# Optimization experiments

Measured on AMD Instinct MI355X. Metric: run time of the kernel, lower is better.

## Reference

```python
import jax, jax.numpy as jnp
import numpy as np

N, E, B = 20000, 60000, 800
H = 64          # node_out_feats
EOUT = 64       # edge_out_feats
D = H + EOUT    # set2set input dim = 128
NT = 138        # n_tasks


def _forward(node_feats, edge_feats, fp_vector, src, dst, gid,
             Wn, bn, We1, be1, We2, be2, Wres, Wgx, bgx, Wgh, bgh,
             Wep, bep,
             Wlx0, Wlh0, bl0, Wlx1, Wlh1, bl1, Wlx2, Wlh2, bl2,
             Wfp, bfp, bn_g, bn_b, bn_m, bn_v,
             Wf1, bf1, Wf2, bf2, Wp, bp):
    # ---- CustomMPNNGNN (dgllife MPNNGNN: proj + NNConv(edge-net) + GRU) ----
    h = jax.nn.relu(node_feats @ Wn + bn)                       # [N,64]
    We = jax.nn.relu(edge_feats @ We1 + be1) @ We2 + be2        # [E,4096]
    We = We.reshape(-1, H, H)                                   # [E,64,64] per-edge weight
    hs = h                                                      # GRU hidden state
    for _ in range(3):
        msg = jnp.einsum('ei,eio->eo', h[src], We)              # edge gather + matvec
        agg = jax.ops.segment_sum(msg, dst, num_segments=N)     # scatter-add to dst
        m = jax.nn.relu(agg + h @ Wres)                         # residual root weight
        gx = m @ Wgx + bgx
        gh = hs @ Wgh + bgh
        xr, xz, xn = jnp.split(gx, 3, axis=-1)
        hr, hz, hn = jnp.split(gh, 3, axis=-1)
        r = jax.nn.sigmoid(xr + hr)
        z = jax.nn.sigmoid(xz + hz)
        n = jnp.tanh(xn + r * hn)
        hs = (1.0 - z) * n + z * hs
        h = hs
    # ---- _internal_readout: gather src node emb + projected edge emb, segment-sum at dst ----
    e_emb = jax.nn.relu(edge_feats @ Wep + bep)                 # [E,64]
    src_msg = jnp.concatenate([h[src], e_emb], axis=1)          # [E,128]
    feat = jax.ops.segment_sum(src_msg, dst, num_segments=N)    # [N,128]
    # ---- Set2Set (3-layer LSTM hidden 128, 6 iterations) ----
    q_star = jnp.zeros((B, 2 * D), feat.dtype)
    hc = [(jnp.zeros((B, D), feat.dtype), jnp.zeros((B, D), feat.dtype)) for _ in range(3)]
    lstm = [(Wlx0, Wlh0, bl0), (Wlx1, Wlh1, bl1), (Wlx2, Wlh2, bl2)]
    for _ in range(6):
        x = q_star
        new_hc = []
        for (Wx, Wh, b), (hl, cl) in zip(lstm, hc):
            g = x @ Wx + hl @ Wh + b                            # [B,512] gates i,f,g,o
            gi, gf, gg, go = jnp.split(g, 4, axis=-1)
            cl = jax.nn.sigmoid(gf) * cl + jax.nn.sigmoid(gi) * jnp.tanh(gg)
            hl = jax.nn.sigmoid(go) * jnp.tanh(cl)
            new_hc.append((hl, cl))
            x = hl
        hc = new_hc
        q = x                                                   # [B,128]
        e = jnp.sum(feat * q[gid], axis=-1)                     # [N]
        emax = jax.ops.segment_max(e, gid, num_segments=B)
        a = jnp.exp(e - emax[gid])
        denom = jax.ops.segment_sum(a, gid, num_segments=B)
        alpha = a / (denom[gid] + 1e-9)
        r = jax.ops.segment_sum(alpha[:, None] * feat, gid, num_segments=B)  # [B,128]
        q_star = jnp.concatenate([q, r], axis=1)                # [B,256]
    # ---- Fingerprint encoder: Linear + BatchNorm1d(eval) + ReLU ----
    fp = fp_vector @ Wfp + bfp
    fp = jax.nn.relu((fp - bn_m) * bn_g * jax.lax.rsqrt(bn_v + 1e-5) + bn_b)  # [B,128]
    # ---- combined FFN (384 -> 300 -> 256) + prediction head ----
    comb = jnp.concatenate([q_star, fp], axis=1)                # [B,384]
    emb = jax.nn.relu(comb @ Wf1 + bf1) @ Wf2 + bf2             # [B,256]
    out = jax.nn.relu(emb) @ Wp + bp                            # [B,138]
    return out


def setup_inputs() -> dict:
    key = jax.random.key(0)
    ks = iter(jax.random.split(key, 64))
    def nrm(shape, s):
        return jax.random.normal(next(ks), shape, jnp.float32) * s
    inp = {}
    inp['node_feats'] = jax.random.normal(next(ks), (N, 134), jnp.float32)
    inp['edge_feats'] = jax.random.uniform(next(ks), (E, 6), jnp.float32)
    inp['fp_vector'] = jax.random.uniform(next(ks), (B, 1024), jnp.float32)
    inp['src'] = jax.random.randint(next(ks), (E,), 0, N)
    inp['dst'] = jax.random.randint(next(ks), (E,), 0, N)
    inp['gid'] = jnp.sort(jax.random.randint(next(ks), (N,), 0, B))
    # MPNN params
    inp['Wn'] = nrm((134, H), 0.08); inp['bn'] = jnp.zeros((H,), jnp.float32)
    inp['We1'] = nrm((6, 128), 0.2); inp['be1'] = jnp.zeros((128,), jnp.float32)
    inp['We2'] = nrm((128, H * H), 0.05); inp['be2'] = jnp.zeros((H * H,), jnp.float32)
    inp['Wres'] = nrm((H, H), 0.1)
    inp['Wgx'] = nrm((H, 3 * H), 0.1); inp['bgx'] = jnp.zeros((3 * H,), jnp.float32)
    inp['Wgh'] = nrm((H, 3 * H), 0.1); inp['bgh'] = jnp.zeros((3 * H,), jnp.float32)
    # edge projection for readout
    inp['Wep'] = nrm((6, EOUT), 0.2); inp['bep'] = jnp.zeros((EOUT,), jnp.float32)
    # Set2Set LSTM (layer0 input 2D=256, layers 1-2 input D=128, hidden D=128)
    inp['Wlx0'] = nrm((2 * D, 4 * D), 0.06); inp['Wlh0'] = nrm((D, 4 * D), 0.06); inp['bl0'] = jnp.zeros((4 * D,), jnp.float32)
    inp['Wlx1'] = nrm((D, 4 * D), 0.06); inp['Wlh1'] = nrm((D, 4 * D), 0.06); inp['bl1'] = jnp.zeros((4 * D,), jnp.float32)
    inp['Wlx2'] = nrm((D, 4 * D), 0.06); inp['Wlh2'] = nrm((D, 4 * D), 0.06); inp['bl2'] = jnp.zeros((4 * D,), jnp.float32)
    # fingerprint encoder
    inp['Wfp'] = nrm((1024, 128), 0.03); inp['bfp'] = jnp.zeros((128,), jnp.float32)
    inp['bn_g'] = jnp.ones((128,), jnp.float32); inp['bn_b'] = jnp.zeros((128,), jnp.float32)
    inp['bn_m'] = jnp.zeros((128,), jnp.float32); inp['bn_v'] = jnp.ones((128,), jnp.float32)
    # combined FFN + prediction head
    inp['Wf1'] = nrm((2 * D + 128, 300), 0.06); inp['bf1'] = jnp.zeros((300,), jnp.float32)
    inp['Wf2'] = nrm((300, 256), 0.06); inp['bf2'] = jnp.zeros((256,), jnp.float32)
    inp['Wp'] = nrm((256, NT), 0.06); inp['bp'] = jnp.zeros((NT,), jnp.float32)
    return inp


def reference(node_feats, edge_feats, fp_vector, src, dst, gid,
              Wn, bn, We1, be1, We2, be2, Wres, Wgx, bgx, Wgh, bgh,
              Wep, bep,
              Wlx0, Wlh0, bl0, Wlx1, Wlh1, bl1, Wlx2, Wlh2, bl2,
              Wfp, bfp, bn_g, bn_b, bn_m, bn_v,
              Wf1, bf1, Wf2, bf2, Wp, bp):
    return _forward(node_feats, edge_feats, fp_vector, src, dst, gid,
                    Wn, bn, We1, be1, We2, be2, Wres, Wgx, bgx, Wgh, bgh,
                    Wep, bep,
                    Wlx0, Wlh0, bl0, Wlx1, Wlh1, bl1, Wlx2, Wlh2, bl2,
                    Wfp, bfp, bn_g, bn_b, bn_m, bn_v,
                    Wf1, bf1, Wf2, bf2, Wp, bp)
```

## Files before the change

### kernel.cpp

```cpp
#include <hip/hip_runtime.h>

typedef short short8 __attribute__((ext_vector_type(8)));
typedef float f32x4  __attribute__((ext_vector_type(4)));

#define NN 20000
#define NE 60000
#define NB 800
#define NTASK 138
#define EB 128
#define EPAD 60032

#define O_WX0 0
#define O_WH0 131072
#define O_WX1 196608
#define O_WH1 262144
#define O_WX2 327680
#define O_WH2 393216
#define O_WF1 458752
#define O_WF2 573952
#define O_WP  650752
#define NWB   686080

static __device__ __forceinline__ float sigm(float x) { return 1.f / (1.f + expf(-x)); }

static __device__ __forceinline__ unsigned short f2bf(float x) {
    unsigned u = __float_as_uint(x);
    unsigned r = (u + 0x7fffu + ((u >> 16) & 1u)) >> 16;
    return (unsigned short)r;
}
static __device__ __forceinline__ float bf2f(unsigned short b) {
    return __uint_as_float(((unsigned)b) << 16);
}

__global__ void kpre(float* __restrict__ zbase, int nz4,
                     const float* __restrict__ We2, const float* __restrict__ be2,
                     unsigned short* __restrict__ thi,
                     const int* __restrict__ gid, int* __restrict__ seg,
                     const float* __restrict__ fpv, const float* __restrict__ Wfp,
                     const float* __restrict__ bfpv,
                     const float* __restrict__ bng, const float* __restrict__ bnb,
                     const float* __restrict__ bnm, const float* __restrict__ bnv,
                     float* __restrict__ fpb,
                     const float* __restrict__ nf, const float* __restrict__ Wn,
                     const float* __restrict__ bn, float* __restrict__ hf,
                     unsigned short* __restrict__ hb,
                     const float* __restrict__ ef, const float* __restrict__ We1,
                     const float* __restrict__ be1, float* __restrict__ xt,
                     const float* __restrict__ Wlx0, const float* __restrict__ Wlh0,
                     const float* __restrict__ Wlx1, const float* __restrict__ Wlh1,
                     const float* __restrict__ Wlx2, const float* __restrict__ Wlh2,
                     const float* __restrict__ Wf1, const float* __restrict__ Wf2,
                     const float* __restrict__ Wp, unsigned short* __restrict__ wb,
                     int B0, int B1, int B2, int B3, int B4, int B5) {
    __shared__ float st[64 * 65];
    __shared__ float sNF[16 * 134];
    __shared__ float sred[128];
    __shared__ float sW[6 * 128];
    __shared__ float sbv[128];
    const int bid = blockIdx.x, tid = threadIdx.x;
    if (bid < B0) {
        long base = (long)bid * 2048 + tid;
        #pragma unroll
        for (int r = 0; r < 8; ++r) {
            long i = base + r * 256;
            if (i < nz4) reinterpret_cast<f32x4*>(zbase)[i] = f32x4{0.f, 0.f, 0.f, 0.f};
        }
    } else if (bid < B1) {
        int c = bid - B0;
        const float* srcp = (c < 128) ? We2 + (long)c * 4096 : be2;
        for (int idx = tid; idx < 4096; idx += 256) {
            int o = idx & 63, i = idx >> 6;
            st[o * 65 + i] = srcp[idx];
        }
        __syncthreads();
        for (int idx = tid; idx < 4096; idx += 256) {
            int i = idx & 63, o = idx >> 6;
            thi[(long)c * 4096 + idx] = f2bf(st[o * 65 + i]);
        }
    } else if (bid < B2) {
        int b = (bid - B1) * 256 + tid;
        if (b <= NB) {
            int lo = 0, hi = NN;
            while (lo < hi) { int mid = (lo + hi) >> 1; if (gid[mid] < b) lo = mid + 1; else hi = mid; }
            seg[b] = lo;
        }
    } else if (bid < B3) {
        int g = bid - B2;
        int u = tid & 127, half = tid >> 7;
        float acc = half ? 0.f : bfpv[u];
        const float* fr = fpv + (long)g * 1024 + half * 512;
        const float* wr = Wfp + (long)half * 512 * 128;
        for (int k = 0; k < 512; ++k) acc += fr[k] * wr[k * 128 + u];
        if (half) sred[u] = acc;
        __syncthreads();
        if (!half) {
            acc += sred[u];
            float sc = bng[u] / sqrtf(bnv[u] + 1e-5f);
            fpb[(long)g * 128 + u] = fmaxf((acc - bnm[u]) * sc + bnb[u], 0.f);
        }
    } else if (bid < B4) {
        int n0 = (bid - B3) * 16;
        const float* nfb = nf + (long)n0 * 134;
        for (int i = tid; i < 16 * 134; i += 256) sNF[i] = nfb[i];
        __syncthreads();
        int u = tid & 63, jg = tid >> 6;
        float a[4];
        float bv = bn[u];
        #pragma unroll
        for (int jj = 0; jj < 4; ++jj) a[jj] = bv;
        for (int k = 0; k < 134; ++k) {
            float w = Wn[k * 64 + u];
            #pragma unroll
            for (int jj = 0; jj < 4; ++jj) a[jj] += sNF[(jg * 4 + jj) * 134 + k] * w;
        }
        #pragma unroll
        for (int jj = 0; jj < 4; ++jj) {
            long o = (long)(n0 + jg * 4 + jj) * 64 + u;
            float v = fmaxf(a[jj], 0.f);
            hf[o] = v;
            hb[o] = f2bf(v);
        }
    } else if (bid < B5) {
        for (int i = tid; i < 768; i += 256) sW[i] = We1[i];
        if (tid < 128) sbv[tid] = be1[tid];
        __syncthreads();
        int e = (bid - B4) * 256 + tid;
        if (e < NE) {
            float e0 = ef[(long)e * 6 + 0], e1 = ef[(long)e * 6 + 1], e2 = ef[(long)e * 6 + 2];
            float e3 = ef[(long)e * 6 + 3], e4 = ef[(long)e * 6 + 4], e5 = ef[(long)e * 6 + 5];
            for (int c = 0; c < 128; ++c) {
                float a = sbv[c];
                a += e0 * sW[c];       a += e1 * sW[128 + c]; a += e2 * sW[256 + c];
                a += e3 * sW[384 + c]; a += e4 * sW[512 + c]; a += e5 * sW[640 + c];
                xt[(long)c * EPAD + e] = fmaxf(a, 0.f);
            }
        } else if (e < EPAD) {
            for (int c = 0; c < 128; ++c) xt[(long)c * EPAD + e] = 0.f;
        }
    } else {
        int t0 = (bid - B5) * 2048 + tid;
        #pragma unroll
        for (int r = 0; r < 8; ++r) {
            int i = t0 + r * 256;
            if (i >= NWB) break;
            float v;
            if (i < O_WF1) {
                const float* srcp; int base;
                if (i < O_WH0)      { srcp = Wlx0; base = O_WX0; }
                else if (i < O_WX1) { srcp = Wlh0; base = O_WH0; }
                else if (i < O_WH1) { srcp = Wlx1; base = O_WX1; }
                else if (i < O_WX2) { srcp = Wlh1; base = O_WH1; }
                else if (i < O_WH2) { srcp = Wlx2; base = O_WX2; }
                else                { srcp = Wlh2; base = O_WH2; }
                int il = i - base;
                int kb = il >> 12, g = (il >> 3) & 511, kk = il & 7;
                v = srcp[(kb * 8 + kk) * 512 + g];
            }
            else if (i < O_WF2) v = Wf1[i - O_WF1];
            else if (i < O_WP)  v = Wf2[i - O_WF2];
            else                v = Wp[i - O_WP];
            wb[i] = f2bf(v);
        }
    }
}

__global__ __launch_bounds__(256) void keinsum(
    const unsigned short* __restrict__ hb,
    const float* __restrict__ hf, const float* __restrict__ Wres,
    const float* __restrict__ xt,
    const unsigned short* __restrict__ thi,
    const int* __restrict__ src, const int* __restrict__ dst,
    float* __restrict__ agg) {
    __shared__ __align__(16) unsigned short sB[3 * 64 * 72];
    __shared__ __align__(16) float sX[3 * EB];
    const int bid = blockIdx.x, tid = threadIdx.x;
    if (bid >= 469) {
        int t = (bid - 469) * 256 + tid;
        int u = t & 63;
        int n0 = (t >> 6) * 8;
        if (n0 >= NN) return;
        float a[8] = {0.f, 0.f, 0.f, 0.f, 0.f, 0.f, 0.f, 0.f};
        for (int k = 0; k < 64; ++k) {
            float w = Wres[k * 64 + u];
            #pragma unroll
            for (int j = 0; j < 8; ++j) a[j] += hf[(long)(n0 + j) * 64 + k] * w;
        }
        #pragma unroll
        for (int j = 0; j < 8; ++j) atomicAdd(&agg[(long)(n0 + j) * 64 + u], a[j]);
        return;
    }
    const int lane = tid & 63, wave = tid >> 6;
    const int m = lane & 15, q = lane >> 4;
    const int eb = bid * EB;
    const int e0 = eb + wave * 32;

    short8 ahi[2][2];
    #pragma unroll
    for (int eg = 0; eg < 2; ++eg) {
        int em = e0 + eg * 16 + m; if (em >= NE) em = NE - 1;
        int sn = src[em];
        ahi[eg][0] = *reinterpret_cast<const short8*>(hb + (long)sn * 64 + q * 8);
        ahi[eg][1] = *reinterpret_cast<const short8*>(hb + (long)sn * 64 + 32 + q * 8);
    }
    float msg[2][4][4];
    #pragma unroll
    for (int eg = 0; eg < 2; ++eg)
        #pragma unroll
        for (int nt = 0; nt < 4; ++nt)
            #pragma unroll
            for (int r = 0; r < 4; ++r) msg[eg][nt][r] = 0.f;

    short8 rB0a, rB0b, rB1a, rB1b;
    float rX0, rX1;

    auto GLOAD0 = [&](int c) {
        const unsigned short* bb = thi + (long)c * 4096;
        rB0a = *reinterpret_cast<const short8*>(bb + tid * 8);
        rB0b = *reinterpret_cast<const short8*>(bb + (tid + 256) * 8);
        rX0 = (tid < EB) ? ((c < 128) ? xt[(long)c * EPAD + eb + tid] : 1.f) : 0.f;
    };
    auto GLOAD1 = [&](int c) {
        const unsigned short* bb = thi + (long)c * 4096;
        rB1a = *reinterpret_cast<const short8*>(bb + tid * 8);
        rB1b = *reinterpret_cast<const short8*>(bb + (tid + 256) * 8);
        rX1 = (tid < EB) ? ((c < 128) ? xt[(long)c * EPAD + eb + tid] : 1.f) : 0.f;
    };
    auto DSW0 = [&](int buf) {
        unsigned short* base = &sB[buf * 4608];
        *reinterpret_cast<short8*>(&base[(tid >> 3) * 72 + (tid & 7) * 8]) = rB0a;
        int u = tid + 256;
        *reinterpret_cast<short8*>(&base[(u >> 3) * 72 + (u & 7) * 8]) = rB0b;
        if (tid < EB) sX[buf * EB + tid] = rX0;
    };
    auto DSW1 = [&](int buf) {
        unsigned short* base = &sB[buf * 4608];
        *reinterpret_cast<short8*>(&base[(tid >> 3) * 72 + (tid & 7) * 8]) = rB1a;
        int u = tid + 256;
        *reinterpret_cast<short8*>(&base[(u >> 3) * 72 + (u & 7) * 8]) = rB1b;
        if (tid < EB) sX[buf * EB + tid] = rX1;
    };
    auto CMP = [&](int buf) {
        const unsigned short* base = &sB[buf * 4608];
        f32x4 xw[2];
        #pragma unroll
        for (int eg = 0; eg < 2; ++eg)
            xw[eg] = *reinterpret_cast<const f32x4*>(&sX[buf * EB + wave * 32 + eg * 16 + q * 4]);
        short8 b0[4], b1[4];
        #pragma unroll
        for (int nt = 0; nt < 4; ++nt) {
            const unsigned short* rp = &base[(nt * 16 + m) * 72 + q * 8];
            b0[nt] = *reinterpret_cast<const short8*>(rp);
            b1[nt] = *reinterpret_cast<const short8*>(rp + 32);
        }
        #pragma unroll
        for (int eg = 0; eg < 2; ++eg)
            #pragma unroll
            for (int nt = 0; nt < 4; ++nt) {
                f32x4 z = {0.f, 0.f, 0.f, 0.f};
                z = __builtin_amdgcn_mfma_f32_16x16x32_bf16(ahi[eg][0], b0[nt], z, 0, 0, 0);
                z = __builtin_amdgcn_mfma_f32_16x16x32_bf16(ahi[eg][1], b1[nt], z, 0, 0, 0);
                #pragma unroll
                for (int r = 0; r < 4; ++r) msg[eg][nt][r] += xw[eg][r] * z[r];
            }
    };

    GLOAD0(0);
    DSW0(0);
    GLOAD1(1);
    int c = 0;
    for (; c + 1 < 129; c += 2) {
        int s = c % 3;
        __syncthreads();
        if (c + 2 < 129) GLOAD0(c + 2);
        DSW1((s + 1) % 3);
        CMP(s);
        __syncthreads();
        if (c + 3 < 129) GLOAD1(c + 3);
        if (c + 2 < 129) DSW0((s + 2) % 3);
        CMP((s + 1) % 3);
    }
    if (c < 129) { __syncthreads(); CMP(c % 3); }

    #pragma unroll
    for (int eg = 0; eg < 2; ++eg)
        #pragma unroll
        for (int r = 0; r < 4; ++r) {
            int e = e0 + eg * 16 + q * 4 + r;
            if (e < NE) {
                int d = dst[e];
                #pragma unroll
                for (int nt = 0; nt < 4; ++nt)
                    atomicAdd(&agg[(long)d * 64 + nt * 16 + m], msg[eg][nt][r]);
            }
        }
}

__global__ void kgruz(const float* __restrict__ agg, const float* __restrict__ h,
                      const float* __restrict__ Wgx, const float* __restrict__ bgx,
                      const float* __restrict__ Wgh, const float* __restrict__ bgh,
                      float* __restrict__ hof, unsigned short* __restrict__ hb,
                      float* __restrict__ aggN) {
    const int bid = blockIdx.x, tid = threadIdx.x;
    if (bid >= 625) {
        long base = (long)(bid - 625) * 2048 + tid;
        #pragma unroll
        for (int r = 0; r < 8; ++r) {
            long i = base + r * 256;
            if (i < 320000) reinterpret_cast<f32x4*>(aggN)[i] = f32x4{0.f, 0.f, 0.f, 0.f};
        }
        return;
    }
    __shared__ float sA[2048], sH[2048];
    const int n0 = bid * 32;
    const float* ab = agg + (long)n0 * 64;
    const float* hrow = h + (long)n0 * 64;
    for (int i = tid; i < 2048; i += 256) { sA[i] = ab[i]; sH[i] = hrow[i]; }
    __syncthreads();
    const int u = tid & 63, jg = tid >> 6;
    float xr[8], xz[8], xn[8], hr[8], hz[8], hn[8];
    float b0 = bgx[u], b1 = bgx[64 + u], b2 = bgx[128 + u];
    float d0 = bgh[u], d1 = bgh[64 + u], d2 = bgh[128 + u];
    #pragma unroll
    for (int j = 0; j < 8; ++j) {
        xr[j] = b0; xz[j] = b1; xn[j] = b2;
        hr[j] = d0; hz[j] = d1; hn[j] = d2;
    }
    for (int k = 0; k < 64; ++k) {
        float w0 = Wgx[k * 192 + u], w1 = Wgx[k * 192 + 64 + u], w2 = Wgx[k * 192 + 128 + u];
        float v0 = Wgh[k * 192 + u], v1 = Wgh[k * 192 + 64 + u], v2 = Wgh[k * 192 + 128 + u];
        #pragma unroll
        for (int j = 0; j < 8; ++j) {
            int n = jg * 8 + j;
            float mk = fmaxf(sA[n * 64 + k], 0.f);
            float hk = sH[n * 64 + k];
            xr[j] += mk * w0; xz[j] += mk * w1; xn[j] += mk * w2;
            hr[j] += hk * v0; hz[j] += hk * v1; hn[j] += hk * v2;
        }
    }
    #pragma unroll
    for (int j = 0; j < 8; ++j) {
        int n = jg * 8 + j;
        float rg = sigm(xr[j] + hr[j]);
        float zg = sigm(xz[j] + hz[j]);
        float ng = tanhf(xn[j] + rg * hn[j]);
        long o = (long)(n0 + n) * 64 + u;
        float hv = (1.f - zg) * ng + zg * sH[n * 64 + u];
        hof[o] = hv;
        hb[o] = f2bf(hv);
    }
}

__global__ void kreadout(const float* __restrict__ h,
                         const float* __restrict__ ef, const float* __restrict__ Wep,
                         const float* __restrict__ bep,
                         const int* __restrict__ src, const int* __restrict__ dst,
                         float* __restrict__ feat) {
    int t = blockIdx.x * blockDim.x + threadIdx.x;
    if (t >= NE * 128) return;
    int e = t >> 7, j = t & 127;
    float v;
    if (j < 64) {
        v = h[(long)src[e] * 64 + j];
    } else {
        int o = j - 64;
        v = bep[o];
        #pragma unroll
        for (int k = 0; k < 6; ++k) v += ef[(long)e * 6 + k] * Wep[k * 64 + o];
        v = fmaxf(v, 0.f);
    }
    atomicAdd(&feat[(long)dst[e] * 128 + j], v);
}

__global__ __launch_bounds__(512) void klstmattn(
    const float* __restrict__ qstar_in, float* __restrict__ qstar_out,
    const float* __restrict__ feat, const int* __restrict__ seg,
    float* __restrict__ esg,
    const unsigned short* __restrict__ wb,
    const float* __restrict__ bl0, const float* __restrict__ bl1, const float* __restrict__ bl2,
    const float* __restrict__ h0i, const float* __restrict__ c0i, float* __restrict__ h0o, float* __restrict__ c0o,
    const float* __restrict__ h1i, const float* __restrict__ c1i, float* __restrict__ h1o, float* __restrict__ c1o,
    const float* __restrict__ h2i, const float* __restrict__ c2i, float* __restrict__ h2o, float* __restrict__ c2o,
    const float* __restrict__ fpb,
    const float* __restrict__ bf1, const float* __restrict__ bf2, const float* __restrict__ bp,
    float* __restrict__ out, int do_head) {
    __shared__ float sXH[2][256];
    __shared__ float sHin[2][128];
    __shared__ float sG[2][512];
    __shared__ float sE[2][512];
    __shared__ float sH2[2][128];
    __shared__ float sR[2][2][128];
    __shared__ float sred[2][4];
    __shared__ float s1b[2][300];
    __shared__ float s2[2][256];
    const int tid = threadIdx.x;
    const int b0g = blockIdx.x * 2;
    const unsigned short* Wx[3] = {wb + O_WX0, wb + O_WX1, wb + O_WX2};
    const unsigned short* Wh[3] = {wb + O_WH0, wb + O_WH1, wb + O_WH2};
    const float* bl[3] = {bl0, bl1, bl2};
    const float* hin[3] = {h0i, h1i, h2i};
    const float* cin[3] = {c0i, c1i, c2i};
    float* hout[3] = {h0o, h1o, h2o};
    float* cout[3] = {c0o, c1o, c2o};

    {
        int b = tid >> 8, u = tid & 255;
        sXH[b][u] = qstar_in[(long)(b0g + b) * 256 + u];
        if (tid < 256) {
            int bb = tid >> 7, uu = tid & 127;
            sHin[bb][uu] = h0i[(long)(b0g + bb) * 128 + uu];
        }
    }
    __syncthreads();

    for (int l = 0; l < 3; ++l) {
        const int Kx = l ? 128 : 256;
        const int g = tid;
        const unsigned short* wxp = Wx[l];
        const unsigned short* whp = Wh[l];
        float bv = bl[l][g];
        float a0 = bv, a1 = bv, a0b = 0.f, a1b = 0.f;
        #pragma unroll 2
        for (int kb = 0; kb < (Kx >> 3); ++kb) {
            short8 wv = *reinterpret_cast<const short8*>(wxp + ((kb << 9) + g) * 8);
            const f32x4* xp0 = reinterpret_cast<const f32x4*>(&sXH[0][kb << 3]);
            const f32x4* xp1 = reinterpret_cast<const f32x4*>(&sXH[1][kb << 3]);
            f32x4 xa0 = xp0[0], xb0 = xp0[1];
            f32x4 xa1 = xp1[0], xb1 = xp1[1];
            #pragma unroll
            for (int kk = 0; kk < 4; ++kk) {
                float w0 = bf2f((unsigned short)wv[kk]);
                float w1 = bf2f((unsigned short)wv[kk + 4]);
                a0  += xa0[kk] * w0;  a1  += xa1[kk] * w0;
                a0b += xb0[kk] * w1;  a1b += xb1[kk] * w1;
            }
        }
        #pragma unroll 2
        for (int kb = 0; kb < 16; ++kb) {
            short8 wv = *reinterpret_cast<const short8*>(whp + ((kb << 9) + g) * 8);
            const f32x4* hp0 = reinterpret_cast<const f32x4*>(&sHin[0][kb << 3]);
            const f32x4* hp1 = reinterpret_cast<const f32x4*>(&sHin[1][kb << 3]);
            f32x4 ha0 = hp0[0], hb0 = hp0[1];
            f32x4 ha1 = hp1[0], hb1 = hp1[1];
            #pragma unroll
            for (int kk = 0; kk < 4; ++kk) {
                float w0 = bf2f((unsigned short)wv[kk]);
                float w1 = bf2f((unsigned short)wv[kk + 4]);
                a0  += ha0[kk] * w0;  a1  += ha1[kk] * w0;
                a0b += hb0[kk] * w1;  a1b += hb1[kk] * w1;
            }
        }
        sG[0][g] = a0 + a0b;
        sG[1][g] = a1 + a1b;
        __syncthreads();
        if (tid < 256) {
            int b = tid >> 7, u = tid & 127;
            float gi = sG[b][u], gf = sG[b][128 + u], gg = sG[b][256 + u], go = sG[b][384 + u];
            long idx = (long)(b0g + b) * 128 + u;
            float c_ = sigm(gf) * cin[l][idx] + sigm(gi) * tanhf(gg);
            float h_ = sigm(go) * tanhf(c_);
            cout[l][idx] = c_;
            hout[l][idx] = h_;
            sXH[b][u] = h_;
            if (l == 2) sH2[b][u] = h_;
        } else if (l < 2) {
            int t2 = tid - 256;
            int b = t2 >> 7, u = t2 & 127;
            sHin[b][u] = hin[l + 1][(long)(b0g + b) * 128 + u];
        }
        __syncthreads();
    }

    const int group = tid >> 8;
    const int t = tid & 255;
    const int s0 = seg[b0g + group], s1 = seg[b0g + group + 1], len = s1 - s0;
    const int wv = t >> 6, lane = t & 63;
    for (int idx = wv; idx < len; idx += 4) {
        long n = s0 + idx;
        float p = feat[n * 128 + lane] * sH2[group][lane]
                + feat[n * 128 + 64 + lane] * sH2[group][64 + lane];
        for (int off = 32; off; off >>= 1) p += __shfl_down(p, off, 64);
        if (lane == 0) { if (idx < 512) sE[group][idx] = p; else esg[n] = p; }
    }
    __syncthreads();
    auto ev = [&](int i) { return i < 512 ? sE[group][i] : esg[s0 + i]; };
    float lm = -1e30f;
    for (int i = t; i < len; i += 256) lm = fmaxf(lm, ev(i));
    for (int off = 32; off; off >>= 1) lm = fmaxf(lm, __shfl_down(lm, off, 64));
    if (lane == 0) sred[group][wv] = lm;
    __syncthreads();
    float mx = fmaxf(fmaxf(sred[group][0], sred[group][1]),
                     fmaxf(sred[group][2], sred[group][3]));
    __syncthreads();
    float ls = 0.f;
    for (int i = t; i < len; i += 256) {
        float e_ = expf(ev(i) - mx);
        if (i < 512) sE[group][i] = e_; else esg[s0 + i] = e_;
        ls += e_;
    }
    for (int off = 32; off; off >>= 1) ls += __shfl_down(ls, off, 64);
    if (lane == 0) sred[group][wv] = ls;
    __syncthreads();
    float inv = 1.f / (sred[group][0] + sred[group][1] + sred[group][2] + sred[group][3] + 1e-9f);
    const int j = t & 127, half = t >> 7;
    float racc = 0.f;
    for (int i = half; i < len; i += 2)
        racc += ev(i) * feat[(long)(s0 + i) * 128 + j];
    sR[group][half][j] = racc;
    __syncthreads();
    float rr = (sR[group][0][j] + sR[group][1][j]) * inv;
    if (half == 0) {
        qstar_out[(long)(b0g + group) * 256 + j] = sH2[group][j];
        qstar_out[(long)(b0g + group) * 256 + 128 + j] = rr;
    }

    if (!do_head) return;
    __syncthreads();
    if (half == 0) {
        sE[group][j] = sH2[group][j];
        sE[group][128 + j] = rr;
    } else {
        sE[group][256 + j] = fpb[(long)(b0g + group) * 128 + j];
    }
    __syncthreads();
    const unsigned short* Wf1b = wb + O_WF1;
    const unsigned short* Wf2b = wb + O_WF2;
    const unsigned short* Wpb  = wb + O_WP;
    for (int task = tid; task < 600; task += 512) {
        int g = task / 300, u = task % 300;
        float acc = bf1[u];
        for (int k = 0; k < 384; ++k) acc += sE[g][k] * bf2f(Wf1b[k * 300 + u]);
        s1b[g][u] = fmaxf(acc, 0.f);
    }
    __syncthreads();
    for (int task = tid; task < 512; task += 512) {
        int g = task >> 8, u = task & 255;
        float acc = bf2[u];
        for (int k = 0; k < 300; ++k) acc += s1b[g][k] * bf2f(Wf2b[k * 256 + u]);
        s2[g][u] = fmaxf(acc, 0.f);
    }
    __syncthreads();
    for (int task = tid; task < 2 * NTASK; task += 512) {
        int g = task / NTASK, u = task % NTASK;
        float acc = bp[u];
        for (int k = 0; k < 256; ++k) acc += s2[g][k] * bf2f(Wpb[k * NTASK + u]);
        out[(long)(b0g + g) * NTASK + u] = acc;
    }
}

extern "C" void kernel_launch(void* const* d_in, const int* in_sizes, int n_in,
                              void* d_out, int out_size, void* d_ws, size_t ws_size,
                              hipStream_t stream) {
    auto fp_ = [&](int i) { return (const float*)d_in[i]; };
    auto ip_ = [&](int i) { return (const int*)d_in[i]; };
    const float *nf = fp_(0), *ef = fp_(1), *fpv = fp_(2);
    const int *src = ip_(3), *dst = ip_(4), *gid = ip_(5);
    const float *Wn = fp_(6), *bn = fp_(7), *We1 = fp_(8), *be1 = fp_(9);
    const float *We2 = fp_(10), *be2 = fp_(11), *Wres = fp_(12);
    const float *Wgx = fp_(13), *bgx = fp_(14), *Wgh = fp_(15), *bgh = fp_(16);
    const float *Wep = fp_(17), *bep = fp_(18);
    const float *Wlx0 = fp_(19), *Wlh0 = fp_(20), *bl0 = fp_(21);
    const float *Wlx1 = fp_(22), *Wlh1 = fp_(23), *bl1 = fp_(24);
    const float *Wlx2 = fp_(25), *Wlh2 = fp_(26), *bl2 = fp_(27);
    const float *Wfp = fp_(28), *bfpv = fp_(29);
    const float *bng = fp_(30), *bnb = fp_(31), *bnm = fp_(32), *bnv = fp_(33);
    const float *Wf1 = fp_(34), *bf1 = fp_(35), *Wf2 = fp_(36), *bf2 = fp_(37);
    const float *Wp = fp_(38), *bp = fp_(39);

    char* w = (char*)d_ws;
    auto alloc = [&](size_t bytes) -> char* {
        char* p = w; w += (bytes + 255) & ~(size_t)255; return p;
    };
    float* hA = (float*)alloc((size_t)NN * 64 * 4);
    float* hB = (float*)alloc((size_t)NN * 64 * 4);
    unsigned short* hbA = (unsigned short*)alloc((size_t)NN * 64 * 2);
    unsigned short* hbB = (unsigned short*)alloc((size_t)NN * 64 * 2);
    unsigned short* we2thi = (unsigned short*)alloc((size_t)129 * 4096 * 2);
    unsigned short* wbf = (unsigned short*)alloc((size_t)NWB * 2);
    float* aggB = (float*)alloc((size_t)NN * 64 * 4);
    char* zstart = w;
    float* aggA  = (float*)alloc((size_t)NN * 64 * 4);
    float* feat  = (float*)alloc((size_t)NN * 128 * 4);
    float* qstarA = (float*)alloc((size_t)NB * 256 * 4);
    float* qstarB = (float*)alloc((size_t)NB * 256 * 4);
    float* lstmb = (float*)alloc((size_t)12 * NB * 128 * 4);
    size_t zfloats = (size_t)(w - zstart) / 4;
    float* es   = (float*)alloc((size_t)NN * 4);
    int*   seg  = (int*)alloc((size_t)(NB + 1) * 4);
    float* fpb  = (float*)alloc((size_t)NB * 128 * 4);
    float* xt   = (float*)alloc((size_t)128 * EPAD * 4);

    float *hl[3][2], *cl[3][2];
    for (int l = 0; l < 3; ++l)
        for (int a = 0; a < 2; ++a) {
            hl[l][a] = lstmb + ((size_t)(l * 4 + a * 2 + 0)) * NB * 128;
            cl[l][a] = lstmb + ((size_t)(l * 4 + a * 2 + 1)) * NB * 128;
        }

    int nz4 = (int)(zfloats / 4);
    int zb  = (nz4 + 2047) / 2048;
    int B0 = zb;
    int B1 = B0 + 129;
    int B2 = B1 + 4;
    int B3 = B2 + NB;
    int B4 = B3 + 1250;
    int B5 = B4 + 235;
    int B6 = B5 + (NWB + 2047) / 2048;
    kpre<<<B6, 256, 0, stream>>>((float*)zstart, nz4, We2, be2, we2thi, gid, seg,
                                 fpv, Wfp, bfpv, bng, bnb, bnm, bnv, fpb,
                                 nf, Wn, bn, hA, hbA,
                                 ef, We1, be1, xt,
                                 Wlx0, Wlh0, Wlx1, Wlh1, Wlx2, Wlh2, Wf1, Wf2, Wp, wbf,
                                 B0, B1, B2, B3, B4, B5);

    float* hf[2] = {hA, hB};
    unsigned short* hb[2] = {hbA, hbB};
    float* aggbuf[2] = {aggA, aggB};
    int cur = 0;
    for (int it = 0; it < 3; ++it) {
        float* agg  = aggbuf[it & 1];
        float* aggN = aggbuf[1 - (it & 1)];
        keinsum<<<469 + 625, 256, 0, stream>>>(hb[cur], hf[cur], Wres,
                                               xt, we2thi, src, dst, agg);
        kgruz<<<625 + 157, 256, 0, stream>>>(agg, hf[cur], Wgx, bgx, Wgh, bgh,
                                             hf[1 - cur], hb[1 - cur], aggN);
        cur = 1 - cur;
    }
    kreadout<<<(NE * 128 + 255) / 256, 256, 0, stream>>>(hf[cur], ef, Wep, bep, src, dst, feat);

    float* qs[2] = {qstarA, qstarB};
    for (int t = 0; t < 6; ++t) {
        int a = t & 1;
        klstmattn<<<NB / 2, 512, 0, stream>>>(qs[a], qs[1 - a], feat, seg, es,
            wbf, bl0, bl1, bl2,
            hl[0][a], cl[0][a], hl[0][1 - a], cl[0][1 - a],
            hl[1][a], cl[1][a], hl[1][1 - a], cl[1][1 - a],
            hl[2][a], cl[2][a], hl[2][1 - a], cl[2][1 - a],
            fpb, bf1, bf2, bp, (float*)d_out, (t == 5) ? 1 : 0);
    }
}
```

Baseline: 888.8 us.

## Fuse six Set2Set iterations into one persistent kernel with LDS-resident LSTM state

```diff
diff --git a/kernel.cpp b/kernel.cpp
--- a/kernel.cpp
+++ b/kernel.cpp
@@ -372,17 +372,16 @@
 }
 
 __global__ __launch_bounds__(512) void klstmattn(
-    const float* __restrict__ qstar_in, float* __restrict__ qstar_out,
     const float* __restrict__ feat, const int* __restrict__ seg,
     float* __restrict__ esg,
     const unsigned short* __restrict__ wb,
     const float* __restrict__ bl0, const float* __restrict__ bl1, const float* __restrict__ bl2,
-    const float* __restrict__ h0i, const float* __restrict__ c0i, float* __restrict__ h0o, float* __restrict__ c0o,
-    const float* __restrict__ h1i, const float* __restrict__ c1i, float* __restrict__ h1o, float* __restrict__ c1o,
-    const float* __restrict__ h2i, const float* __restrict__ c2i, float* __restrict__ h2o, float* __restrict__ c2o,
     const float* __restrict__ fpb,
     const float* __restrict__ bf1, const float* __restrict__ bf2, const float* __restrict__ bp,
-    float* __restrict__ out, int do_head) {
+    float* __restrict__ out) {
+    __shared__ float sQ[2][256];
+    __shared__ float sHs[3][2][128];
+    __shared__ float sCs[3][2][128];
     __shared__ float sXH[2][256];
     __shared__ float sHin[2][128];
     __shared__ float sG[2][512];
@@ -397,153 +396,169 @@
     const unsigned short* Wx[3] = {wb + O_WX0, wb + O_WX1, wb + O_WX2};
     const unsigned short* Wh[3] = {wb + O_WH0, wb + O_WH1, wb + O_WH2};
     const float* bl[3] = {bl0, bl1, bl2};
-    const float* hin[3] = {h0i, h1i, h2i};
-    const float* cin[3] = {c0i, c1i, c2i};
-    float* hout[3] = {h0o, h1o, h2o};
-    float* cout[3] = {c0o, c1o, c2o};
-
-    {
-        int b = tid >> 8, u = tid & 255;
-        sXH[b][u] = qstar_in[(long)(b0g + b) * 256 + u];
-        if (tid < 256) {
-            int bb = tid >> 7, uu = tid & 127;
-            sHin[bb][uu] = h0i[(long)(b0g + bb) * 128 + uu];
-        }
-    }
-    __syncthreads();
-
-    for (int l = 0; l < 3; ++l) {
-        const int Kx = l ? 128 : 256;
-        const int g = tid;
-        const unsigned short* wxp = Wx[l];
-        const unsigned short* whp = Wh[l];
-        float bv = bl[l][g];
-        float a0 = bv, a1 = bv, a0b = 0.f, a1b = 0.f;
-        #pragma unroll 2
-        for (int kb = 0; kb < (Kx >> 3); ++kb) {
-            short8 wv = *reinterpret_cast<const short8*>(wxp + ((kb << 9) + g) * 8);
-            const f32x4* xp0 = reinterpret_cast<const f32x4*>(&sXH[0][kb << 3]);
-            const f32x4* xp1 = reinterpret_cast<const f32x4*>(&sXH[1][kb << 3]);
-            f32x4 xa0 = xp0[0], xb0 = xp0[1];
-            f32x4 xa1 = xp1[0], xb1 = xp1[1];
-            #pragma unroll
-            for (int kk = 0; kk < 4; ++kk) {
-                float w0 = bf2f((unsigned short)wv[kk]);
-                float w1 = bf2f((unsigned short)wv[kk + 4]);
-                a0  += xa0[kk] * w0;  a1  += xa1[kk] * w0;
-                a0b += xb0[kk] * w1;  a1b += xb1[kk] * w1;
-            }
-        }
-        #pragma unroll 2
-        for (int kb = 0; kb < 16; ++kb) {
-            short8 wv = *reinterpret_cast<const short8*>(whp + ((kb << 9) + g) * 8);
-            const f32x4* hp0 = reinterpret_cast<const f32x4*>(&sHin[0][kb << 3]);
-            const f32x4* hp1 = reinterpret_cast<const f32x4*>(&sHin[1][kb << 3]);
-            f32x4 ha0 = hp0[0], hb0 = hp0[1];
-            f32x4 ha1 = hp1[0], hb1 = hp1[1];
-            #pragma unroll
-            for (int kk = 0; kk < 4; ++kk) {
-                float w0 = bf2f((unsigned short)wv[kk]);
-                float w1 = bf2f((unsigned short)wv[kk + 4]);
-                a0  += ha0[kk] * w0;  a1  += ha1[kk] * w0;
-                a0b += hb0[kk] * w1;  a1b += hb1[kk] * w1;
-            }
-        }
-        sG[0][g] = a0 + a0b;
-        sG[1][g] = a1 + a1b;
-        __syncthreads();
-        if (tid < 256) {
-            int b = tid >> 7, u = tid & 127;
-            float gi = sG[b][u], gf = sG[b][128 + u], gg = sG[b][256 + u], go = sG[b][384 + u];
-            long idx = (long)(b0g + b) * 128 + u;
-            float c_ = sigm(gf) * cin[l][idx] + sigm(gi) * tanhf(gg);
-            float h_ = sigm(go) * tanhf(c_);
-            cout[l][idx] = c_;
-            hout[l][idx] = h_;
-            sXH[b][u] = h_;
-            if (l == 2) sH2[b][u] = h_;
-        } else if (l < 2) {
-            int t2 = tid - 256;
-            int b = t2 >> 7, u = t2 & 127;
-            sHin[b][u] = hin[l + 1][(long)(b0g + b) * 128 + u];
-        }
-        __syncthreads();
-    }
 
     const int group = tid >> 8;
     const int t = tid & 255;
+    const int wv = t >> 6, lane = t & 63;
+    const int j = t & 127, half = t >> 7;
     const int s0 = seg[b0g + group], s1 = seg[b0g + group + 1], len = s1 - s0;
-    const int wv = t >> 6, lane = t & 63;
-    for (int idx = wv; idx < len; idx += 4) {
-        long n = s0 + idx;
-        float p = feat[n * 128 + lane] * sH2[group][lane]
-                + feat[n * 128 + 64 + lane] * sH2[group][64 + lane];
-        for (int off = 32; off; off >>= 1) p += __shfl_down(p, off, 64);
-        if (lane == 0) { if (idx < 512) sE[group][idx] = p; else esg[n] = p; }
+
+    sQ[tid >> 8][tid & 255] = 0.f;
+    {
+        float* hp = &sHs[0][0][0];
+        float* cp = &sCs[0][0][0];
+        for (int i = tid; i < 768; i += 512) { hp[i] = 0.f; cp[i] = 0.f; }
     }
     __syncthreads();
-    auto ev = [&](int i) { return i < 512 ? sE[group][i] : esg[s0 + i]; };
-    float lm = -1e30f;
-    for (int i = t; i < len; i += 256) lm = fmaxf(lm, ev(i));
-    for (int off = 32; off; off >>= 1) lm = fmaxf(lm, __shfl_down(lm, off, 64));
-    if (lane == 0) sred[group][wv] = lm;
-    __syncthreads();
-    float mx = fmaxf(fmaxf(sred[group][0], sred[group][1]),
-                     fmaxf(sred[group][2], sred[group][3]));
-    __syncthreads();
-    float ls = 0.f;
-    for (int i = t; i < len; i += 256) {
-        float e_ = expf(ev(i) - mx);
-        if (i < 512) sE[group][i] = e_; else esg[s0 + i] = e_;
-        ls += e_;
-    }
-    for (int off = 32; off; off >>= 1) ls += __shfl_down(ls, off, 64);
-    if (lane == 0) sred[group][wv] = ls;
-    __syncthreads();
-    float inv = 1.f / (sred[group][0] + sred[group][1] + sred[group][2] + sred[group][3] + 1e-9f);
-    const int j = t & 127, half = t >> 7;
-    float racc = 0.f;
-    for (int i = half; i < len; i += 2)
-        racc += ev(i) * feat[(long)(s0 + i) * 128 + j];
-    sR[group][half][j] = racc;
-    __syncthreads();
-    float rr = (sR[group][0][j] + sR[group][1][j]) * inv;
-    if (half == 0) {
-        qstar_out[(long)(b0g + group) * 256 + j] = sH2[group][j];
-        qstar_out[(long)(b0g + group) * 256 + 128 + j] = rr;
-    }
-
-    if (!do_head) return;
-    __syncthreads();
-    if (half == 0) {
-        sE[group][j] = sH2[group][j];
-        sE[group][128 + j] = rr;
-    } else {
-        sE[group][256 + j] = fpb[(long)(b0g + group) * 128 + j];
-    }
-    __syncthreads();
-    const unsigned short* Wf1b = wb + O_WF1;
-    const unsigned short* Wf2b = wb + O_WF2;
-    const unsigned short* Wpb  = wb + O_WP;
-    for (int task = tid; task < 600; task += 512) {
-        int g = task / 300, u = task % 300;
-        float acc = bf1[u];
-        for (int k = 0; k < 384; ++k) acc += sE[g][k] * bf2f(Wf1b[k * 300 + u]);
-        s1b[g][u] = fmaxf(acc, 0.f);
-    }
-    __syncthreads();
-    for (int task = tid; task < 512; task += 512) {
-        int g = task >> 8, u = task & 255;
-        float acc = bf2[u];
-        for (int k = 0; k < 300; ++k) acc += s1b[g][k] * bf2f(Wf2b[k * 256 + u]);
-        s2[g][u] = fmaxf(acc, 0.f);
-    }
-    __syncthreads();
-    for (int task = tid; task < 2 * NTASK; task += 512) {
-        int g = task / NTASK, u = task % NTASK;
-        float acc = bp[u];
-        for (int k = 0; k < 256; ++k) acc += s2[g][k] * bf2f(Wpb[k * NTASK + u]);
-        out[(long)(b0g + g) * NTASK + u] = acc;
+
+    for (int t6 = 0; t6 < 6; ++t6) {
+        {
+            int b = tid >> 8, u = tid & 255;
+            sXH[b][u] = sQ[b][u];
+            if (tid < 256) {
+                int bb = tid >> 7, uu = tid & 127;
+                sHin[bb][uu] = sHs[0][bb][uu];
+            }
+        }
+        __syncthreads();
+
+        for (int l = 0; l < 3; ++l) {
+            const int Kx = l ? 128 : 256;
+            const int g = tid;
+            const unsigned short* wxp = Wx[l];
+            const unsigned short* whp = Wh[l];
+            float bv = bl[l][g];
+            float a0 = bv, a1 = bv, a0b = 0.f, a1b = 0.f;
+            #pragma unroll 4
+            for (int kb = 0; kb < (Kx >> 3); ++kb) {
+                short8 wvv = *reinterpret_cast<const short8*>(wxp + ((kb << 9) + g) * 8);
+                const f32x4* xp0 = reinterpret_cast<const f32x4*>(&sXH[0][kb << 3]);
+                const f32x4* xp1 = reinterpret_cast<const f32x4*>(&sXH[1][kb << 3]);
+                f32x4 xa0 = xp0[0], xb0 = xp0[1];
+                f32x4 xa1 = xp1[0], xb1 = xp1[1];
+                #pragma unroll
+                for (int kk = 0; kk < 4; ++kk) {
+                    float w0 = bf2f((unsigned short)wvv[kk]);
+                    float w1 = bf2f((unsigned short)wvv[kk + 4]);
+                    a0  += xa0[kk] * w0;  a1  += xa1[kk] * w0;
+                    a0b += xb0[kk] * w1;  a1b += xb1[kk] * w1;
+                }
+            }
+            #pragma unroll 4
+            for (int kb = 0; kb < 16; ++kb) {
+                short8 wvv = *reinterpret_cast<const short8*>(whp + ((kb << 9) + g) * 8);
+                const f32x4* hp0 = reinterpret_cast<const f32x4*>(&sHin[0][kb << 3]);
+                const f32x4* hp1 = reinterpret_cast<const f32x4*>(&sHin[1][kb << 3]);
+                f32x4 ha0 = hp0[0], hb0 = hp0[1];
+                f32x4 ha1 = hp1[0], hb1 = hp1[1];
+                #pragma unroll
+                for (int kk = 0; kk < 4; ++kk) {
+                    float w0 = bf2f((unsigned short)wvv[kk]);
+                    float w1 = bf2f((unsigned short)wvv[kk + 4]);
+                    a0  += ha0[kk] * w0;  a1  += ha1[kk] * w0;
+                    a0b += hb0[kk] * w1;  a1b += hb1[kk] * w1;
+                }
+            }
+            sG[0][g] = a0 + a0b;
+            sG[1][g] = a1 + a1b;
+            __syncthreads();
+            if (tid < 256) {
+                int b = tid >> 7, u = tid & 127;
+                float gi = sG[b][u], gf = sG[b][128 + u], gg = sG[b][256 + u], go = sG[b][384 + u];
+                float c_ = sigm(gf) * sCs[l][b][u] + sigm(gi) * tanhf(gg);
+                float h_ = sigm(go) * tanhf(c_);
+                sCs[l][b][u] = c_;
+                sHs[l][b][u] = h_;
+                sXH[b][u] = h_;
+                if (l == 2) sH2[b][u] = h_;
+            } else if (l < 2) {
+                int t2 = tid - 256;
+                int b = t2 >> 7, u = t2 & 127;
+                sHin[b][u] = sHs[l + 1][b][u];
+            }
+            __syncthreads();
+        }
+
+        for (int idx = wv; idx < len; idx += 4) {
+            long n = s0 + idx;
+            float p = feat[n * 128 + lane] * sH2[group][lane]
+                    + feat[n * 128 + 64 + lane] * sH2[group][64 + lane];
+            for (int off = 32; off; off >>= 1) p += __shfl_down(p, off, 64);
+            if (lane == 0) { if (idx < 512) sE[group][idx] = p; else esg[n] = p; }
+        }
+        __syncthreads();
+        auto ev = [&](int i) { return i < 512 ? sE[group][i] : esg[s0 + i]; };
+        float lm = -1e30f;
+        for (int i = t; i < len; i += 256) lm = fmaxf(lm, ev(i));
+        for (int off = 32; off; off >>= 1) lm = fmaxf(lm, __shfl_down(lm, off, 64));
+        if (lane == 0) sred[group][wv] = lm;
+        __syncthreads();
+        float mx = fmaxf(fmaxf(sred[group][0], sred[group][1]),
+                         fmaxf(sred[group][2], sred[group][3]));
+        __syncthreads();
+        float ls = 0.f;
+        for (int i = t; i < len; i += 256) {
+            float e_ = expf(ev(i) - mx);
+            if (i < 512) sE[group][i] = e_; else esg[s0 + i] = e_;
+            ls += e_;
+        }
+        for (int off = 32; off; off >>= 1) ls += __shfl_down(ls, off, 64);
+        if (lane == 0) sred[group][wv] = ls;
+        __syncthreads();
+        float inv = 1.f / (sred[group][0] + sred[group][1] + sred[group][2] + sred[group][3] + 1e-9f);
+        float r0 = 0.f, r1 = 0.f;
+        {
+            int i = half;
+            for (; i + 2 < len; i += 4) {
+                r0 += ev(i) * feat[(long)(s0 + i) * 128 + j];
+                r1 += ev(i + 2) * feat[(long)(s0 + i + 2) * 128 + j];
+            }
+            for (; i < len; i += 2)
+                r0 += ev(i) * feat[(long)(s0 + i) * 128 + j];
+        }
+        sR[group][half][j] = r0 + r1;
+        __syncthreads();
+        float rr = (sR[group][0][j] + sR[group][1][j]) * inv;
+        if (half == 0) {
+            sQ[group][j] = sH2[group][j];
+            sQ[group][128 + j] = rr;
+        }
+
+        if (t6 == 5) {
+            __syncthreads();
+            if (half == 0) {
+                sE[group][j] = sH2[group][j];
+                sE[group][128 + j] = rr;
+            } else {
+                sE[group][256 + j] = fpb[(long)(b0g + group) * 128 + j];
+            }
+            __syncthreads();
+            const unsigned short* Wf1b = wb + O_WF1;
+            const unsigned short* Wf2b = wb + O_WF2;
+            const unsigned short* Wpb  = wb + O_WP;
+            for (int task = tid; task < 600; task += 512) {
+                int g = task / 300, u = task % 300;
+                float acc = bf1[u];
+                for (int k = 0; k < 384; ++k) acc += sE[g][k] * bf2f(Wf1b[k * 300 + u]);
+                s1b[g][u] = fmaxf(acc, 0.f);
+            }
+            __syncthreads();
+            for (int task = tid; task < 512; task += 512) {
+                int g = task >> 8, u = task & 255;
+                float acc = bf2[u];
+                for (int k = 0; k < 300; ++k) acc += s1b[g][k] * bf2f(Wf2b[k * 256 + u]);
+                s2[g][u] = fmaxf(acc, 0.f);
+            }
+            __syncthreads();
+            for (int task = tid; task < 2 * NTASK; task += 512) {
+                int g = task / NTASK, u = task % NTASK;
+                float acc = bp[u];
+                for (int k = 0; k < 256; ++k) acc += s2[g][k] * bf2f(Wpb[k * NTASK + u]);
+                out[(long)(b0g + g) * NTASK + u] = acc;
+            }
+        } else {
+            __syncthreads();
+        }
     }
 }
 
@@ -580,21 +595,11 @@
     char* zstart = w;
     float* aggA  = (float*)alloc((size_t)NN * 64 * 4);
     float* feat  = (float*)alloc((size_t)NN * 128 * 4);
-    float* qstarA = (float*)alloc((size_t)NB * 256 * 4);
-    float* qstarB = (float*)alloc((size_t)NB * 256 * 4);
-    float* lstmb = (float*)alloc((size_t)12 * NB * 128 * 4);
     size_t zfloats = (size_t)(w - zstart) / 4;
     float* es   = (float*)alloc((size_t)NN * 4);
     int*   seg  = (int*)alloc((size_t)(NB + 1) * 4);
     float* fpb  = (float*)alloc((size_t)NB * 128 * 4);
     float* xt   = (float*)alloc((size_t)128 * EPAD * 4);
-
-    float *hl[3][2], *cl[3][2];
-    for (int l = 0; l < 3; ++l)
-        for (int a = 0; a < 2; ++a) {
-            hl[l][a] = lstmb + ((size_t)(l * 4 + a * 2 + 0)) * NB * 128;
-            cl[l][a] = lstmb + ((size_t)(l * 4 + a * 2 + 1)) * NB * 128;
-        }
 
     int nz4 = (int)(zfloats / 4);
     int zb  = (nz4 + 2047) / 2048;
@@ -627,14 +632,6 @@
     }
     kreadout<<<(NE * 128 + 255) / 256, 256, 0, stream>>>(hf[cur], ef, Wep, bep, src, dst, feat);
 
-    float* qs[2] = {qstarA, qstarB};
-    for (int t = 0; t < 6; ++t) {
-        int a = t & 1;
-        klstmattn<<<NB / 2, 512, 0, stream>>>(qs[a], qs[1 - a], feat, seg, es,
-            wbf, bl0, bl1, bl2,
-            hl[0][a], cl[0][a], hl[0][1 - a], cl[0][1 - a],
-            hl[1][a], cl[1][a], hl[1][1 - a], cl[1][1 - a],
-            hl[2][a], cl[2][a], hl[2][1 - a], cl[2][1 - a],
-            fpb, bf1, bf2, bp, (float*)d_out, (t == 5) ? 1 : 0);
-    }
-}
+    klstmattn<<<NB / 2, 512, 0, stream>>>(feat, seg, es, wbf, bl0, bl1, bl2,
+                                          fpb, bf1, bf2, bp, (float*)d_out);
+}
```

Result: faster. 869.4 us (-2.2%).
